# Kernel tuning notes

Measured on AMD Instinct MI355X. Metric: run time of the kernel, lower is better.

The kernel has to match this reference:

```python
import jax, jax.numpy as jnp
import numpy as np
import math

R = 3  # search_radius
GROUPS = 4

def _conv(x, w):
    return jax.lax.conv_general_dilated(x, w, (1, 1), 'SAME',
                                        dimension_numbers=('NCHW', 'OIHW', 'NCHW'))

def _gn(x, g, b, eps=1e-5):
    B, C, H, W = x.shape
    xr = x.reshape(B, GROUPS, C // GROUPS, H, W)
    m = xr.mean(axis=(2, 3, 4), keepdims=True)
    v = xr.var(axis=(2, 3, 4), keepdims=True)
    xn = ((xr - m) * jax.lax.rsqrt(v + eps)).reshape(B, C, H, W)
    return xn * g.reshape(1, C, 1, 1) + b.reshape(1, C, 1, 1)

def _gelu(x):
    return jax.nn.gelu(x, approximate=False)

def _encode(x, W0, Ws, G, Bt):
    x = _gelu(_gn(_conv(x, W0), G[0], Bt[0]))
    for i in range(Ws.shape[0]):  # fixed depth-1 layers
        x = _gelu(_gn(_conv(x, Ws[i]), G[i + 1], Bt[i + 1]))
    return x

def _center_w(h, w):
    y = jnp.linspace(-1.0, 1.0, h)
    x = jnp.linspace(-1.0, 1.0, w)
    yy, xx = jnp.meshgrid(y, x, indexing='ij')
    g = jnp.exp(-(yy ** 2 + xx ** 2) / (2 * 0.5 ** 2))
    return (g / g.sum())[None, None]  # [1,1,H,W]

def _l2n(x):  # F.normalize(dim=1, eps=1e-6)
    n = jnp.sqrt(jnp.sum(x * x, axis=1, keepdims=True))
    return x / jnp.maximum(n, 1e-6)

def setup_inputs() -> dict:
    key = jax.random.key(0)
    ks = jax.random.split(key, 24)
    B, Cr, H, W, Ch, MH = 256, 6, 64, 64, 32, 128
    depth = 4
    feat_dim = Ch * 3 + 2
    s = 0.05
    return {
        'rubin_patch': jax.random.normal(ks[0], (B, Cr, H, W), jnp.float32),
        'vis_patch': jax.random.normal(ks[1], (B, 1, H, W), jnp.float32),
        'pixel_to_sky': jax.random.normal(ks[2], (B, 2, 2), jnp.float32),
        'rW0': jax.random.normal(ks[3], (Ch, Cr, 3, 3), jnp.float32) * s,
        'rWs': jax.random.normal(ks[4], (depth - 1, Ch, Ch, 3, 3), jnp.float32) * s,
        'rG': 1.0 + jax.random.normal(ks[5], (depth, Ch), jnp.float32) * s,
        'rBt': jax.random.normal(ks[6], (depth, Ch), jnp.float32) * s,
        'vW0': jax.random.normal(ks[7], (Ch, 1, 3, 3), jnp.float32) * s,
        'vWs': jax.random.normal(ks[8], (depth - 1, Ch, Ch, 3, 3), jnp.float32) * s,
        'vG': 1.0 + jax.random.normal(ks[9], (depth, Ch), jnp.float32) * s,
        'vBt': jax.random.normal(ks[10], (depth, Ch), jnp.float32) * s,
        'projR': jax.random.normal(ks[11], (Ch, Ch), jnp.float32) * s,
        'projV': jax.random.normal(ks[12], (Ch, Ch), jnp.float32) * s,
        'log_temp': jnp.array(math.log(0.05), jnp.float32),
        'W1': jax.random.normal(ks[13], (feat_dim, MH), jnp.float32) * s,
        'b1': jax.random.normal(ks[14], (MH,), jnp.float32) * s,
        'W2': jax.random.normal(ks[15], (MH, MH), jnp.float32) * s,
        'b2': jax.random.normal(ks[16], (MH,), jnp.float32) * s,
        'W3': jax.random.normal(ks[17], (MH, 3), jnp.float32) * s,
        'b3': jax.random.normal(ks[18], (3,), jnp.float32) * s,
    }

def _forward(rubin_patch, vis_patch, pixel_to_sky, rW0, rWs, rG, rBt,
             vW0, vWs, vG, vBt, projR, projV, log_temp,
             W1, b1, W2, b2, W3, b3):
    rubin_feat = _encode(rubin_patch, rW0, rWs, rG, rBt)  # [B,C,H,W]
    vis_feat = _encode(vis_patch, vW0, vWs, vG, vBt)
    B, C, H, W = rubin_feat.shape

    # --- weighted cross-correlation cost volume ---
    rubin_n = _l2n(jnp.einsum('oc,bchw->bohw', projR, rubin_feat))
    vis_n = _l2n(jnp.einsum('oc,bchw->bohw', projV, vis_feat))
    rubin_energy = jnp.sum(rubin_n * rubin_n, axis=1, keepdims=True)
    gauss = _center_w(H, W)
    sw = rubin_energy * gauss
    sw = sw / (jnp.sum(sw, axis=(2, 3), keepdims=True) + 1e-8)
    rw = rubin_n * sw  # fold weights into rubin features once
    vis_pad = jnp.pad(vis_n, ((0, 0), (0, 0), (R, R), (R, R)), mode='edge')
    scale = 1.0 / math.sqrt(float(C))
    logits = []
    for dy in range(-R, R + 1):
        for dx in range(-R, R + 1):
            sh = vis_pad[:, :, R + dy:R + dy + H, R + dx:R + dx + W]
            logits.append(jnp.sum(rw * sh, axis=(1, 2, 3)) * scale)
    logits = jnp.stack(logits, axis=1)  # [B,(2R+1)^2]

    dx_lut = jnp.array([float(dx) for dy in range(-R, R + 1) for dx in range(-R, R + 1)], jnp.float32)
    dy_lut = jnp.array([float(dy) for dy in range(-R, R + 1) for dx in range(-R, R + 1)], jnp.float32)
    temp = jnp.maximum(jnp.exp(log_temp), 1e-3)
    probs = jax.nn.softmax(logits / temp, axis=1)
    coarse_dx = jnp.sum(probs * dx_lut[None], axis=1)
    coarse_dy = jnp.sum(probs * dy_lut[None], axis=1)

    # --- center-biased pooling + MLP refine ---
    rp = jnp.sum(rubin_feat * gauss, axis=(2, 3))  # [B,C]
    vp = jnp.sum(vis_feat * gauss, axis=(2, 3))
    pooled = jnp.concatenate([rp, vp, rp - vp,
                              jnp.stack([coarse_dx, coarse_dy], axis=1)], axis=1)
    h = _gelu(pooled @ W1 + b1)
    h = _gelu(h @ W2 + b2)
    res = h @ W3 + b3  # [B,3]

    dx_px = coarse_dx + res[:, 0]
    dy_px = coarse_dy + res[:, 1]
    log_sigma = jnp.clip(res[:, 2], -6.0, 3.0)
    pix = jnp.stack([dx_px, dy_px], axis=1)
    pred_sky = jnp.einsum('bij,bj->bi', pixel_to_sky, pix)
    # pack all differentiable outputs: [dx, dy, pred_sky(2), log_sigma, logits(49)]
    return jnp.concatenate([dx_px[:, None], dy_px[:, None], pred_sky,
                            log_sigma[:, None], logits], axis=1)  # [B,54]

def reference(rubin_patch, vis_patch, pixel_to_sky, rW0, rWs, rG, rBt,
              vW0, vWs, vG, vBt, projR, projV, log_temp,
              W1, b1, W2, b2, W3, b3):
    return _forward(rubin_patch, vis_patch, pixel_to_sky, rW0, rWs, rG, rBt,
                    vW0, vWs, vG, vBt, projR, projV, log_temp,
                    W1, b1, W2, b2, W3, b3)
```

## Files before the change

### kernel.cpp

```cpp
#include <hip/hip_runtime.h>
#include <math.h>

#define HW 4096
#define NB 256

typedef __attribute__((ext_vector_type(8))) short bf16x8_t;
typedef __attribute__((ext_vector_type(16))) float f32x16_t;

__device__ __forceinline__ float gelu_f(float x) {
    float z = x * 0.70710678118654752440f;
    float az = fabsf(z);
    float t = 1.0f / fmaf(0.3275911f, az, 1.0f);
    float p = t * fmaf(t, fmaf(t, fmaf(t, fmaf(t, 1.061405429f, -1.453152027f),
                                       1.421413741f), -0.284496736f), 0.254829592f);
    float e = __expf(-az * az);
    float er = 1.0f - p * e;
    er = copysignf(er, z);
    return 0.5f * x * (1.0f + er);
}
__device__ __forceinline__ unsigned short f2bf(float f) {
    unsigned int u = __float_as_uint(f);
    unsigned int r = u + 0x7FFFu + ((u >> 16) & 1u);
    return (unsigned short)(r >> 16);
}
__device__ __forceinline__ float bf2f(unsigned short h) {
    return __uint_as_float(((unsigned int)h) << 16);
}


__global__ __launch_bounds__(256) void gauss_kernel(float* __restrict__ gauss) {
    __shared__ float sg[HW];
    __shared__ float sR[4];
    int tid = threadIdx.x;
    float part = 0.0f;
    for (int p = tid; p < HW; p += 256) {
        int y = p >> 6, x = p & 63;
        float yy = -1.0f + (2.0f / 63.0f) * (float)y;
        float xx = -1.0f + (2.0f / 63.0f) * (float)x;
        float g = expf(-(yy * yy + xx * xx) * 2.0f);
        sg[p] = g;
        part += g;
    }
#pragma unroll
    for (int off = 32; off > 0; off >>= 1) part += __shfl_down(part, off);
    if ((tid & 63) == 0) sR[tid >> 6] = part;
    __syncthreads();
    float invt = 1.0f / (sR[0] + sR[1] + sR[2] + sR[3]);
    for (int p = tid; p < HW; p += 256) gauss[p] = sg[p] * invt;
}

__global__ __launch_bounds__(256) void prep_w_kernel(
    const float* __restrict__ rWs, const float* __restrict__ vWs,
    const float* __restrict__ rW0, const float* __restrict__ vW0,
    const float* __restrict__ projR, const float* __restrict__ projV,
    unsigned short* __restrict__ wq) {
    int i = blockIdx.x * 256 + threadIdx.x;
    if (i >= 119808) return;
    float wv;
    if (i < 110592) {
        int j = i & 7;
        int lane = (i >> 3) & 63;
        int f = i >> 9;
        int hl = f & 1, k2 = (f >> 1) & 1, tap = (f >> 2) % 9, layer = (f >> 2) / 9;
        int co = lane & 31, hf = lane >> 5;
        int ci = k2 * 16 + hf * 8 + j;
        int ky = tap / 3, kx = tap % 3;
        wv = (layer < 3)
            ? rWs[(((size_t)layer * 32 + co) * 32 + ci) * 9 + ky * 3 + kx]
            : vWs[(((size_t)(layer - 3) * 32 + co) * 32 + ci) * 9 + ky * 3 + kx];
        unsigned short h = f2bf(wv);
        unsigned short l = f2bf(wv - bf2f(h));
        wq[i] = hl ? l : h;
        return;
    }
    if (i < 115712) {
        int i2 = i - 110592;
        int j = i2 & 7;
        int lane = (i2 >> 3) & 63;
        int co = lane & 31, hf = lane >> 5;
        if (i2 < 4096) {
            int f = i2 >> 9;
            int hl = f & 1, ks = f >> 1;
            int q = ks * 16 + hf * 8 + j;
            wv = (q < 54) ? rW0[((size_t)co * 6 + q / 9) * 9 + q % 9] : 0.0f;
            unsigned short h = f2bf(wv);
            unsigned short l = f2bf(wv - bf2f(h));
            wq[i] = hl ? l : h;
        } else {
            int i3 = i2 - 4096;
            int f = i3 >> 9;
            int q = hf * 8 + j;
            wv = (q < 9) ? vW0[(size_t)co * 9 + q] : 0.0f;
            unsigned short h = f2bf(wv);
            unsigned short l = f2bf(wv - bf2f(h));
            wq[i] = f ? l : h;
        }
        return;
    }
    int i4 = i - 115712;
    const float* pw = (i4 < 2048) ? projR : projV;
    int r = i4 & 2047;
    int j = r & 7;
    int lane = (r >> 3) & 63;
    int f = r >> 9;
    int hl = f & 1, k2 = f >> 1;
    int co = lane & 31, hf = lane >> 5;
    int ci = k2 * 16 + hf * 8 + j;
    wv = pw[(size_t)co * 32 + ci];
    unsigned short h = f2bf(wv);
    unsigned short l = f2bf(wv - bf2f(h));
    wq[i] = hl ? l : h;
}

template <int CIN>
__global__ __launch_bounds__(128) void conv_first_m_kernel(
    const float* __restrict__ in, const unsigned short* __restrict__ wq0,
    unsigned short* __restrict__ qout, float* __restrict__ statp) {
    constexpr int KQ = CIN * 9;
    constexpr int KS = (KQ + 15) / 16;
    const int b = blockIdx.y;
    const int strip = blockIdx.x;
    const int tid = threadIdx.x;
    const int wv = tid >> 6;
    const int lane = tid & 63;
    const int m = lane & 31;
    const int hf = lane >> 5;
    const int xh32 = wv * 32;

    __shared__ __align__(16) char smem[20736];
    __shared__ float sRed[2][8];
    float* sInF = (float*)smem;

    const int y0 = strip * 4;
    const float* inb = in + (size_t)b * CIN * HW;
    for (int idx = tid; idx < CIN * 6 * 66; idx += 128) {
        int ci = idx / 396;
        int rem = idx - ci * 396;
        int r = rem / 66;
        int col = rem - r * 66;
        int gy = y0 - 1 + r;
        int gx = col - 1;
        float v = 0.0f;
        if (gy >= 0 && gy < 64 && gx >= 0 && gx < 64) v = inb[ci * HW + gy * 64 + gx];
        sInF[ci * 396 + r * 66 + col] = v;
    }

    int P[KS][8];
#pragma unroll
    for (int ks = 0; ks < KS; ++ks)
#pragma unroll
        for (int j = 0; j < 8; ++j) {
            int q = ks * 16 + hf * 8 + j;
            int ci = q / 9, tap = q - ci * 9;
            int ky = tap / 3, kx = tap - ky * 3;
            P[ks][j] = (q < KQ) ? (ci * 396 + ky * 66 + kx) : 0;
        }
    bf16x8_t Wf[KS][2];
#pragma unroll
    for (int ks = 0; ks < KS; ++ks)
#pragma unroll
        for (int hl = 0; hl < 2; ++hl)
            Wf[ks][hl] = __builtin_bit_cast(
                bf16x8_t, *(const uint4*)(wq0 + (size_t)(ks * 2 + hl) * 512 + lane * 8));
    __syncthreads();

    f32x16_t acc[4];
#pragma unroll
    for (int i = 0; i < 4; ++i)
#pragma unroll
        for (int j = 0; j < 16; ++j) acc[i][j] = 0.0f;

    const int xcol = xh32 + m;
#pragma unroll
    for (int orow = 0; orow < 4; ++orow) {
        const int obase = orow * 66 + xcol;
#pragma unroll
        for (int ks = 0; ks < KS; ++ks) {
            unsigned int pk[4];
#pragma unroll
            for (int e = 0; e < 4; ++e) {
                float v0 = sInF[P[ks][e * 2] + obase];
                float v1 = sInF[P[ks][e * 2 + 1] + obase];
                pk[e] = (unsigned)f2bf(v0) | ((unsigned)f2bf(v1) << 16);
            }
            uint4 u; u.x = pk[0]; u.y = pk[1]; u.z = pk[2]; u.w = pk[3];
            bf16x8_t A = __builtin_bit_cast(bf16x8_t, u);
            acc[orow] = __builtin_amdgcn_mfma_f32_32x32x16_bf16(A, Wf[ks][0], acc[orow], 0, 0, 0);
            acc[orow] = __builtin_amdgcn_mfma_f32_32x32x16_bf16(A, Wf[ks][1], acc[orow], 0, 0, 0);
        }
    }

    __syncthreads();
    unsigned short* lds_t = (unsigned short*)smem;
    const int co = lane & 31;
    float s1 = 0.0f, s2 = 0.0f;
#pragma unroll
    for (int orow = 0; orow < 4; ++orow) {
#pragma unroll
        for (int r = 0; r < 16; ++r) {
            int mm = (r & 3) + 8 * (r >> 2) + 4 * hf;
            int pxl = (orow << 6) + xh32 + mm;
            float v = acc[orow][r];
            s1 += v;
            s2 = fmaf(v, v, s2);
            lds_t[pxl * 40 + co] = f2bf(v);
        }
    }
    s1 += __shfl_xor(s1, 32); s2 += __shfl_xor(s2, 32);
    s1 += __shfl_xor(s1, 1);  s2 += __shfl_xor(s2, 1);
    s1 += __shfl_xor(s1, 2);  s2 += __shfl_xor(s2, 2);
    s1 += __shfl_xor(s1, 4);  s2 += __shfl_xor(s2, 4);
    if (lane < 32 && (lane & 7) == 0) {
        sRed[wv][co >> 3] = s1;
        sRed[wv][4 + (co >> 3)] = s2;
    }
    __syncthreads();
    if (tid < 8) statp[((size_t)b * 16 + strip) * 8 + tid] = sRed[0][tid] + sRed[1][tid];

    char* qb = (char*)qout + (size_t)b * 4 * HW * 16;
    const int p0 = y0 * 64;
#pragma unroll
    for (int pi = 0; pi < 2; ++pi) {
        int p = pi * 128 + tid;
#pragma unroll
        for (int s = 0; s < 4; ++s) {
            uint4 uh = *(const uint4*)(lds_t + p * 40 + s * 8);
            *(uint4*)(qb + ((size_t)(s * HW) + p0 + p) * 16) = uh;
        }
    }
}

__global__ __launch_bounds__(256) void gn_finalize_kernel(
    const float* __restrict__ statp, const float* __restrict__ gma,
    const float* __restrict__ bta, float* __restrict__ coef, int n, int ns) {
    int i = blockIdx.x * 256 + threadIdx.x;
    if (i >= n) return;
    int b = i >> 5, c = i & 31, g = c >> 3;
    float s1 = 0.0f, s2 = 0.0f;
    for (int s = 0; s < ns; ++s) {
        s1 += statp[((size_t)b * 16 + s) * 8 + g];
        s2 += statp[((size_t)b * 16 + s) * 8 + 4 + g];
    }
    const float invN = 1.0f / 32768.0f;
    float mean = s1 * invN;
    float var = s2 * invN - mean * mean;
    float rstd = rsqrtf(var + 1e-5f);
    float a = rstd * gma[c];
    float bb = bta[c] - mean * a;
    coef[i * 2 + 0] = a;
    coef[i * 2 + 1] = bb;
}

#define SLOT 80
#define ROWB (66 * SLOT)
__global__ __launch_bounds__(256) void convm_kernel(
    const unsigned short* __restrict__ qin, const float* __restrict__ coef,
    const unsigned short* __restrict__ wq,
    unsigned short* __restrict__ qout, float* __restrict__ statp) {
    const int b = blockIdx.y;
    const int strip = blockIdx.x;
    const int tid = threadIdx.x;
    const int wv = tid >> 6;
    const int lane = tid & 63;
    const int m = lane & 31;
    const int hf = lane >> 5;

    __shared__ __align__(16) char sQ[10 * ROWB];
    __shared__ float sRed[4][8];
    __shared__ float sc[64];

    const int y0 = strip * 8;
    const char* img = (const char*)qin + (size_t)b * 4 * HW * 16;

    if (tid < 64) sc[tid] = coef[b * 64 + tid];
    if (tid < 80) {
        int r = tid >> 3, side = (tid >> 2) & 1, sub = tid & 3;
        uint4 z; z.x = z.y = z.z = z.w = 0;
        *(uint4*)(sQ + r * ROWB + side * 65 * SLOT + sub * 16) = z;
    }
    __syncthreads();

    const int px = tid & 63;
    const int s_id = tid >> 6;
    const int rot = px & 3;
    float ca[8], cb[8];
#pragma unroll
    for (int e = 0; e < 8; ++e) {
        ca[e] = sc[(s_id * 8 + e) * 2 + 0];
        cb[e] = sc[(s_id * 8 + e) * 2 + 1];
    }
    uint4 ld[10];
#pragma unroll
    for (int r = 0; r < 10; ++r) {
        int gy = y0 - 1 + r;
        if (gy >= 0 && gy < 64) {
            ld[r] = *(const uint4*)(img + ((size_t)(s_id * HW) + gy * 64 + px) * 16);
        } else {
            ld[r].x = ld[r].y = ld[r].z = ld[r].w = 0;
        }
    }
    char* dstc = sQ + (px + 1) * SLOT + ((s_id + rot) & 3) * 16;
#pragma unroll
    for (int r = 0; r < 10; ++r) {
        unsigned int hd[4] = {ld[r].x, ld[r].y, ld[r].z, ld[r].w};
        unsigned int ho[4];
#pragma unroll
        for (int e = 0; e < 4; ++e) {
            float x0 = bf2f((unsigned short)(hd[e] & 0xFFFF));
            float x1 = bf2f((unsigned short)(hd[e] >> 16));
            float y0v = gelu_f(fmaf(ca[e * 2], x0, cb[e * 2]));
            float y1v = gelu_f(fmaf(ca[e * 2 + 1], x1, cb[e * 2 + 1]));
            ho[e] = (unsigned)f2bf(y0v) | ((unsigned)f2bf(y1v) << 16);
        }
        uint4 oh; oh.x = ho[0]; oh.y = ho[1]; oh.z = ho[2]; oh.w = ho[3];
        *(uint4*)(dstc + r * ROWB) = oh;
    }
    __syncthreads();

    const int rq = wv & 1;
    const int xh32 = (wv >> 1) * 32;
    f32x16_t acc[4];
#pragma unroll
    for (int i = 0; i < 4; ++i)
#pragma unroll
        for (int j = 0; j < 16; ++j) acc[i][j] = 0.0f;

    for (int kx = 0; kx < 3; ++kx) {
        bf16x8_t Wf[3][2];
#pragma unroll
        for (int ky = 0; ky < 3; ++ky)
#pragma unroll
            for (int k2 = 0; k2 < 2; ++k2) {
                int fi = (((ky * 3 + kx) * 2 + k2) * 2);
                Wf[ky][k2] = __builtin_bit_cast(
                    bf16x8_t, *(const uint4*)(wq + (size_t)fi * 512 + lane * 8));
            }
        const int slotb = xh32 + kx + m;
        const int prot = (m + kx + 3) & 3;
#pragma unroll
        for (int li = 0; li < 6; ++li) {
            const char* rowp = sQ + (rq * 4 + li) * ROWB + slotb * SLOT;
            bf16x8_t Ah[2];
#pragma unroll
            for (int k2 = 0; k2 < 2; ++k2) {
                int s = k2 * 2 + hf;
                Ah[k2] = __builtin_bit_cast(bf16x8_t, *(const uint4*)(rowp + ((s + prot) & 3) * 16));
            }
#pragma unroll
            for (int ky = 0; ky < 3; ++ky) {
                int orow = li - ky;
                if (orow < 0 || orow > 3) continue;
#pragma unroll
                for (int k2 = 0; k2 < 2; ++k2)
                    acc[orow] = __builtin_amdgcn_mfma_f32_32x32x16_bf16(Ah[k2], Wf[ky][k2], acc[orow], 0, 0, 0);
            }
        }
    }

    __syncthreads();
    unsigned short* lds_t = (unsigned short*)sQ;
    const int co = lane & 31;
    float s1 = 0.0f, s2 = 0.0f;
#pragma unroll
    for (int orow = 0; orow < 4; ++orow) {
#pragma unroll
        for (int r = 0; r < 16; ++r) {
            int mm = (r & 3) + 8 * (r >> 2) + 4 * hf;
            int pxl = (rq * 4 + orow) * 64 + xh32 + mm;
            float v = acc[orow][r];
            s1 += v;
            s2 = fmaf(v, v, s2);
            lds_t[pxl * 40 + co] = f2bf(v);
        }
    }
    s1 += __shfl_xor(s1, 32); s2 += __shfl_xor(s2, 32);
    s1 += __shfl_xor(s1, 1);  s2 += __shfl_xor(s2, 1);
    s1 += __shfl_xor(s1, 2);  s2 += __shfl_xor(s2, 2);
    s1 += __shfl_xor(s1, 4);  s2 += __shfl_xor(s2, 4);
    if (lane < 32 && (lane & 7) == 0) {
        sRed[wv][co >> 3] = s1;
        sRed[wv][4 + (co >> 3)] = s2;
    }
    __syncthreads();
    if (tid < 8)
        statp[((size_t)b * 16 + strip) * 8 + tid] =
            sRed[0][tid] + sRed[1][tid] + sRed[2][tid] + sRed[3][tid];

    char* qb = (char*)qout + (size_t)b * 4 * HW * 16;
    const int p0 = y0 * 64;
#pragma unroll
    for (int pi = 0; pi < 2; ++pi) {
        int p = pi * 256 + tid;
#pragma unroll
        for (int s = 0; s < 4; ++s) {
            uint4 uh = *(const uint4*)(lds_t + p * 40 + s * 8);
            *(uint4*)(qb + ((size_t)(s * HW) + p0 + p) * 16) = uh;
        }
    }
}

__global__ __launch_bounds__(256) void proj_kernel(
    const unsigned short* __restrict__ q, const float* __restrict__ coef,
    const unsigned short* __restrict__ wqp, unsigned short* __restrict__ outn,
    float* __restrict__ poolp, float* __restrict__ E, float* __restrict__ swp,
    const float* __restrict__ gauss, int vpad) {
    int b = blockIdx.y, chunk = blockIdx.x, tid = threadIdx.x;
    const int wv = tid >> 6, lane = tid & 63;
    const int ln = lane & 31, hf = lane >> 5;
    __shared__ float sc[64];
    __shared__ float lds_o[256 * 33];
    __shared__ float poolw[4][32];
    __shared__ float sR[4];
    if (tid < 64) sc[tid] = coef[b * 64 + tid];
    __syncthreads();

    const char* qb = (const char*)q + (size_t)b * 4 * HW * 16;
    const int pb0 = chunk * 256 + wv * 64;

    bf16x8_t Bf[2][2];
#pragma unroll
    for (int k2 = 0; k2 < 2; ++k2)
#pragma unroll
        for (int hl = 0; hl < 2; ++hl)
            Bf[k2][hl] = __builtin_bit_cast(
                bf16x8_t, *(const uint4*)(wqp + (size_t)(k2 * 2 + hl) * 512 + lane * 8));

    float psum[2][8];
#pragma unroll
    for (int k2 = 0; k2 < 2; ++k2)
#pragma unroll
        for (int j = 0; j < 8; ++j) psum[k2][j] = 0.0f;

    f32x16_t acc[2];
#pragma unroll
    for (int i = 0; i < 2; ++i)
#pragma unroll
        for (int j = 0; j < 16; ++j) acc[i][j] = 0.0f;

#pragma unroll
    for (int t = 0; t < 2; ++t) {
        int px = pb0 + t * 32 + ln;
        float g = gauss[px];
#pragma unroll
        for (int k2 = 0; k2 < 2; ++k2) {
            int s = k2 * 2 + hf;
            uint4 uh = *(const uint4*)(qb + ((size_t)(s * HW) + px) * 16);
            unsigned int hd[4] = {uh.x, uh.y, uh.z, uh.w};
            unsigned int ah[4], al[4];
#pragma unroll
            for (int e = 0; e < 4; ++e) {
                int c0 = s * 8 + e * 2;
                float x0 = bf2f((unsigned short)(hd[e] & 0xFFFF));
                float x1 = bf2f((unsigned short)(hd[e] >> 16));
                float f0 = gelu_f(fmaf(sc[c0 * 2], x0, sc[c0 * 2 + 1]));
                float f1 = gelu_f(fmaf(sc[c0 * 2 + 2], x1, sc[c0 * 2 + 3]));
                psum[k2][e * 2] = fmaf(f0, g, psum[k2][e * 2]);
                psum[k2][e * 2 + 1] = fmaf(f1, g, psum[k2][e * 2 + 1]);
                unsigned short h0 = f2bf(f0), h1 = f2bf(f1);
                unsigned short l0 = f2bf(f0 - bf2f(h0)), l1 = f2bf(f1 - bf2f(h1));
                ah[e] = (unsigned)h0 | ((unsigned)h1 << 16);
                al[e] = (unsigned)l0 | ((unsigned)l1 << 16);
            }
            uint4 uah; uah.x = ah[0]; uah.y = ah[1]; uah.z = ah[2]; uah.w = ah[3];
            uint4 ual; ual.x = al[0]; ual.y = al[1]; ual.z = al[2]; ual.w = al[3];
            bf16x8_t Ah = __builtin_bit_cast(bf16x8_t, uah);
            bf16x8_t Al = __builtin_bit_cast(bf16x8_t, ual);
            acc[t] = __builtin_amdgcn_mfma_f32_32x32x16_bf16(Ah, Bf[k2][0], acc[t], 0, 0, 0);
            acc[t] = __builtin_amdgcn_mfma_f32_32x32x16_bf16(Ah, Bf[k2][1], acc[t], 0, 0, 0);
            acc[t] = __builtin_amdgcn_mfma_f32_32x32x16_bf16(Al, Bf[k2][0], acc[t], 0, 0, 0);
        }
    }

#pragma unroll
    for (int t = 0; t < 2; ++t)
#pragma unroll
        for (int r = 0; r < 16; ++r) {
            int mm = (r & 3) + 8 * (r >> 2) + 4 * hf;
            lds_o[(wv * 64 + t * 32 + mm) * 33 + ln] = acc[t][r];
        }

#pragma unroll
    for (int k2 = 0; k2 < 2; ++k2)
#pragma unroll
        for (int j = 0; j < 8; ++j) {
            float v = psum[k2][j];
            v += __shfl_xor(v, 1); v += __shfl_xor(v, 2);
            v += __shfl_xor(v, 4); v += __shfl_xor(v, 8);
            v += __shfl_xor(v, 16);
            psum[k2][j] = v;
        }
    if (ln == 0) {
#pragma unroll
        for (int k2 = 0; k2 < 2; ++k2)
#pragma unroll
            for (int j = 0; j < 8; ++j)
                poolw[wv][k2 * 16 + hf * 8 + j] = psum[k2][j];
    }
    __syncthreads();
    if (tid < 32) {
        float s = poolw[0][tid] + poolw[1][tid] + poolw[2][tid] + poolw[3][tid];
        poolp[((size_t)b * 16 + chunk) * 32 + tid] = s;
    }

    int p = chunk * 256 + tid;
    float o[32];
    float nn = 0.0f;
#pragma unroll
    for (int oo = 0; oo < 32; ++oo) {
        o[oo] = lds_o[tid * 33 + oo];
        nn = fmaf(o[oo], o[oo], nn);
    }
    float n = sqrtf(nn);
    float inv = 1.0f / fmaxf(n, 1e-6f);
    if (vpad) {
        int y = p >> 6, x = p & 63;
        unsigned short* vb_ = outn + (size_t)b * 32 * 4608 + y * 72 + x + 4;
#pragma unroll
        for (int oo = 0; oo < 32; ++oo) {
            unsigned short hv = f2bf(o[oo] * inv);
            unsigned short* row = vb_ + (size_t)oo * 4608;
            row[0] = hv;
            if (x == 0) { row[-4] = hv; row[-3] = hv; row[-2] = hv; row[-1] = hv; }
            if (x == 63) { row[1] = hv; row[2] = hv; row[3] = hv; row[4] = hv; }
        }
    } else {
        unsigned short* obp = outn + (size_t)b * 32 * HW + p;
#pragma unroll
        for (int oo = 0; oo < 32; ++oo) obp[(size_t)oo * HW] = f2bf(o[oo] * inv);
    }

    if (E != nullptr) {
        float e = nn * inv * inv;
        E[(size_t)b * HW + p] = e;
        float wvv = e * gauss[p];
#pragma unroll
        for (int off = 32; off > 0; off >>= 1) wvv += __shfl_down(wvv, off);
        if ((tid & 63) == 0) sR[tid >> 6] = wvv;
        __syncthreads();
        if (tid == 0) swp[b * 16 + chunk] = sR[0] + sR[1] + sR[2] + sR[3];
    }
}

__global__ __launch_bounds__(256) void logits_kernel(
    const unsigned short* __restrict__ rn, const unsigned short* __restrict__ vnp,
    const float* __restrict__ E, const float* __restrict__ swp,
    const float* __restrict__ gauss, float* __restrict__ lgpart) {
    int b = blockIdx.x, cg = blockIdx.y, tid = threadIdx.x;
    __shared__ float sR[4][49];
    float acc[49];
#pragma unroll
    for (int k = 0; k < 49; ++k) acc[k] = 0.0f;
    float ssum = 0.0f;
#pragma unroll
    for (int i = 0; i < 16; ++i) ssum += swp[b * 16 + i];
    const float scale = 0.17677669529663688f / (ssum + 1e-8f);
    const int x0 = (tid & 7) * 8;
    const float* Eb = E + (size_t)b * HW;
#pragma unroll 1
    for (int half = 0; half < 2; ++half) {
        const int y = half * 32 + (tid >> 3);
        const int pbase = y * 64 + x0;
        float4 e0 = *(const float4*)(Eb + pbase);
        float4 e1 = *(const float4*)(Eb + pbase + 4);
        float4 g0 = *(const float4*)(gauss + pbase);
        float4 g1 = *(const float4*)(gauss + pbase + 4);
        float qw[8];
        qw[0] = e0.x * g0.x * scale; qw[1] = e0.y * g0.y * scale;
        qw[2] = e0.z * g0.z * scale; qw[3] = e0.w * g0.w * scale;
        qw[4] = e1.x * g1.x * scale; qw[5] = e1.y * g1.y * scale;
        qw[6] = e1.z * g1.z * scale; qw[7] = e1.w * g1.w * scale;
#pragma unroll 1
        for (int cc = 0; cc < 4; ++cc) {
            int c = cg * 4 + cc;
            const unsigned short* rb = rn + ((size_t)b * 32 + c) * HW;
            uint4 rv = *(const uint4*)(rb + pbase);
            unsigned int rd[4] = {rv.x, rv.y, rv.z, rv.w};
            float r_[8];
            r_[0] = bf2f((unsigned short)(rd[0] & 0xFFFF)) * qw[0];
            r_[1] = bf2f((unsigned short)(rd[0] >> 16)) * qw[1];
            r_[2] = bf2f((unsigned short)(rd[1] & 0xFFFF)) * qw[2];
            r_[3] = bf2f((unsigned short)(rd[1] >> 16)) * qw[3];
            r_[4] = bf2f((unsigned short)(rd[2] & 0xFFFF)) * qw[4];
            r_[5] = bf2f((unsigned short)(rd[2] >> 16)) * qw[5];
            r_[6] = bf2f((unsigned short)(rd[3] & 0xFFFF)) * qw[6];
            r_[7] = bf2f((unsigned short)(rd[3] >> 16)) * qw[7];
            const unsigned short* vplane = vnp + ((size_t)b * 32 + c) * 4608;
#pragma unroll
            for (int dy = 0; dy < 7; ++dy) {
                int ry = y + dy - 3;
                ry = ry < 0 ? 0 : (ry > 63 ? 63 : ry);
                const unsigned short* vp = vplane + ry * 72 + x0;
                uint4 va = *(const uint4*)vp;
                uint4 vb2 = *(const uint4*)(vp + 8);
                unsigned int vd[8] = {va.x, va.y, va.z, va.w, vb2.x, vb2.y, vb2.z, vb2.w};
                float v[16];
#pragma unroll
                for (int j2 = 0; j2 < 8; ++j2) {
                    v[j2 * 2] = bf2f((unsigned short)(vd[j2] & 0xFFFF));
                    v[j2 * 2 + 1] = bf2f((unsigned short)(vd[j2] >> 16));
                }
#pragma unroll
                for (int dx = 0; dx < 7; ++dx)
#pragma unroll
                    for (int j = 0; j < 8; ++j)
                        acc[dy * 7 + dx] = fmaf(r_[j], v[j + dx + 1], acc[dy * 7 + dx]);
            }
        }
    }
#pragma unroll
    for (int k = 0; k < 49; ++k) {
#pragma unroll
        for (int off = 32; off > 0; off >>= 1) acc[k] += __shfl_down(acc[k], off);
    }
    int wid = tid >> 6;
    if ((tid & 63) == 0) {
#pragma unroll
        for (int k = 0; k < 49; ++k) sR[wid][k] = acc[k];
    }
    __syncthreads();
    if (tid < 49)
        lgpart[((size_t)b * 8 + cg) * 49 + tid] =
            sR[0][tid] + sR[1][tid] + sR[2][tid] + sR[3][tid];
}

__global__ __launch_bounds__(128) void head_kernel(
    const float* __restrict__ lg, const float* __restrict__ rpp,
    const float* __restrict__ vpp, const float* __restrict__ p2s,
    const float* __restrict__ log_temp,
    const float* __restrict__ W1, const float* __restrict__ b1,
    const float* __restrict__ W2, const float* __restrict__ b2,
    const float* __restrict__ W3, const float* __restrict__ b3,
    float* __restrict__ out) {
    int b = blockIdx.x, t = threadIdx.x;
    __shared__ float slg[49];
    __shared__ float pooled[98];
    __shared__ float h1[128], h2[128];
    __shared__ float cxy[2];
    __shared__ float res[3];
    const float* lgp = lg + (size_t)b * 8 * 49;
    if (t < 49) {
        float s = 0.0f;
#pragma unroll
        for (int g = 0; g < 8; ++g) s += lgp[g * 49 + t];
        slg[t] = s;
    }
    __syncthreads();
    if (t == 0) {
        float temp = fmaxf(expf(log_temp[0]), 0.001f);
        float invT = 1.0f / temp;
        float m = -1e30f;
        for (int k = 0; k < 49; ++k) m = fmaxf(m, slg[k] * invT);
        float s = 0.0f, pdx = 0.0f, pdy = 0.0f;
        for (int k = 0; k < 49; ++k) {
            float e = expf(slg[k] * invT - m);
            s += e;
            pdx += e * (float)((k % 7) - 3);
            pdy += e * (float)((k / 7) - 3);
        }
        cxy[0] = pdx / s;
        cxy[1] = pdy / s;
    }
    __syncthreads();
    if (t < 32) {
        float a = 0.0f, c = 0.0f;
#pragma unroll
        for (int k = 0; k < 16; ++k) {
            a += rpp[((size_t)b * 16 + k) * 32 + t];
            c += vpp[((size_t)b * 16 + k) * 32 + t];
        }
        pooled[t] = a;
        pooled[32 + t] = c;
        pooled[64 + t] = a - c;
    }
    if (t == 0) {
        pooled[96] = cxy[0];
        pooled[97] = cxy[1];
    }
    __syncthreads();
    float s1 = b1[t];
    for (int i = 0; i < 98; ++i) s1 = fmaf(pooled[i], W1[i * 128 + t], s1);
    h1[t] = gelu_f(s1);
    __syncthreads();
    float s2 = b2[t];
    for (int i = 0; i < 128; ++i) s2 = fmaf(h1[i], W2[i * 128 + t], s2);
    h2[t] = gelu_f(s2);
    __syncthreads();
    if (t < 3) {
        float r = b3[t];
        for (int i = 0; i < 128; ++i) r = fmaf(h2[i], W3[i * 3 + t], r);
        res[t] = r;
    }
    __syncthreads();
    if (t == 0) {
        float dxp = cxy[0] + res[0];
        float dyp = cxy[1] + res[1];
        float ls = fminf(fmaxf(res[2], -6.0f), 3.0f);
        const float* M = p2s + b * 4;
        float* ob = out + b * 54;
        ob[0] = dxp;
        ob[1] = dyp;
        ob[2] = M[0] * dxp + M[1] * dyp;
        ob[3] = M[2] * dxp + M[3] * dyp;
        ob[4] = ls;
    }
    if (t < 49) out[b * 54 + 5 + t] = slg[t];
}

extern "C" void kernel_launch(void* const* d_in, const int* in_sizes, int n_in,
                              void* d_out, int out_size, void* d_ws, size_t ws_size,
                              hipStream_t stream) {
    (void)in_sizes; (void)n_in; (void)out_size;
    const float* rubin = (const float*)d_in[0];
    const float* vis   = (const float*)d_in[1];
    const float* p2s   = (const float*)d_in[2];
    const float* rW0   = (const float*)d_in[3];
    const float* rWs   = (const float*)d_in[4];
    const float* rG    = (const float*)d_in[5];
    const float* rBt   = (const float*)d_in[6];
    const float* vW0   = (const float*)d_in[7];
    const float* vWs   = (const float*)d_in[8];
    const float* vG    = (const float*)d_in[9];
    const float* vBt   = (const float*)d_in[10];
    const float* projR = (const float*)d_in[11];
    const float* projV = (const float*)d_in[12];
    const float* logT  = (const float*)d_in[13];
    const float* W1    = (const float*)d_in[14];
    const float* b1    = (const float*)d_in[15];
    const float* W2    = (const float*)d_in[16];
    const float* b2    = (const float*)d_in[17];
    const float* W3    = (const float*)d_in[18];
    const float* b3    = (const float*)d_in[19];
    float* out = (float*)d_out;

    char* ws = (char*)d_ws;
    size_t off = 0;
    unsigned short* vnB = (unsigned short*)(ws + off); off += (size_t)NB * 32 * 4608 * 2;
    float* gauss  = (float*)(ws + off); off += HW * 4;
    float* statp  = (float*)(ws + off); off += (size_t)NB * 16 * 8 * 4;
    float* coefS  = (float*)(ws + off); off += (size_t)NB * 64 * 4;
    float* swp    = (float*)(ws + off); off += (size_t)NB * 16 * 4;
    float* rpp    = (float*)(ws + off); off += (size_t)NB * 16 * 32 * 4;
    float* vpp    = (float*)(ws + off); off += (size_t)NB * 16 * 32 * 4;
    float* lgbuf  = (float*)(ws + off); off += (size_t)NB * 8 * 49 * 4;
    unsigned short* wq = (unsigned short*)(ws + off); off += 119808ull * 2;
    off = (off + 255) & ~(size_t)255;
    const size_t fixed_bytes = off;
    const size_t perb = 2ull * HW * 64 + HW * 4;
    int BC = 1;
    if (ws_size > fixed_bytes + perb) {
        size_t t = (ws_size - fixed_bytes) / perb;
        BC = t > (size_t)NB ? NB : (int)t;
    }
    unsigned short* Q1 = (unsigned short*)(ws + off);
    unsigned short* Q2 = (unsigned short*)(ws + off + (size_t)BC * HW * 64);
    float* E = (float*)(ws + off + 2ull * BC * HW * 64);
    unsigned short* wq0r = wq + 110592;
    unsigned short* wq0v = wq + 114688;
    unsigned short* wqpR = wq + 115712;
    unsigned short* wqpV = wq + 117760;

    dim3 blk256(256), blk128(128);
    gauss_kernel<<<1, 256, 0, stream>>>(gauss);
    prep_w_kernel<<<468, 256, 0, stream>>>(rWs, vWs, rW0, vW0, projR, projV, wq);

    for (int b0 = 0; b0 < NB; b0 += BC) {
        const int bc = (NB - b0) < BC ? (NB - b0) : BC;
        dim3 cg16(16, bc), cg8(8, bc);
        const int gnblk = (bc * 32 + 255) / 256;
        float* sp = statp + (size_t)b0 * 128;
        float* cS = coefS + (size_t)b0 * 64;

        conv_first_m_kernel<1><<<cg16, blk128, 0, stream>>>(vis + (size_t)b0 * HW, wq0v, Q1, sp);
        gn_finalize_kernel<<<gnblk, 256, 0, stream>>>(sp, vG + 0, vBt + 0, cS, bc * 32, 16);
        convm_kernel<<<cg8, blk256, 0, stream>>>(Q1, cS, wq + 3 * 18432, Q2, sp);
        gn_finalize_kernel<<<gnblk, 256, 0, stream>>>(sp, vG + 32, vBt + 32, cS, bc * 32, 8);
        convm_kernel<<<cg8, blk256, 0, stream>>>(Q2, cS, wq + 4 * 18432, Q1, sp);
        gn_finalize_kernel<<<gnblk, 256, 0, stream>>>(sp, vG + 64, vBt + 64, cS, bc * 32, 8);
        convm_kernel<<<cg8, blk256, 0, stream>>>(Q1, cS, wq + 5 * 18432, Q2, sp);
        gn_finalize_kernel<<<gnblk, 256, 0, stream>>>(sp, vG + 96, vBt + 96, cS, bc * 32, 8);
        proj_kernel<<<cg16, blk256, 0, stream>>>(Q2, cS, wqpV, vnB + (size_t)b0 * 32 * 4608,
                                                 vpp + (size_t)b0 * 512,
                                                 (float*)nullptr, (float*)nullptr, gauss, 1);
    }

    for (int b0 = 0; b0 < NB; b0 += BC) {
        const int bc = (NB - b0) < BC ? (NB - b0) : BC;
        dim3 cg16(16, bc), cg8(8, bc);
        const int gnblk = (bc * 32 + 255) / 256;
        float* sp = statp + (size_t)b0 * 128;
        float* cS = coefS + (size_t)b0 * 64;
        float* sw = swp + (size_t)b0 * 16;
        unsigned short* rnB = Q1;

        conv_first_m_kernel<6><<<cg16, blk128, 0, stream>>>(rubin + (size_t)b0 * 6 * HW, wq0r, Q1, sp);
        gn_finalize_kernel<<<gnblk, 256, 0, stream>>>(sp, rG + 0, rBt + 0, cS, bc * 32, 16);
        convm_kernel<<<cg8, blk256, 0, stream>>>(Q1, cS, wq + 0 * 18432, Q2, sp);
        gn_finalize_kernel<<<gnblk, 256, 0, stream>>>(sp, rG + 32, rBt + 32, cS, bc * 32, 8);
        convm_kernel<<<cg8, blk256, 0, stream>>>(Q2, cS, wq + 1 * 18432, Q1, sp);
        gn_finalize_kernel<<<gnblk, 256, 0, stream>>>(sp, rG + 64, rBt + 64, cS, bc * 32, 8);
        convm_kernel<<<cg8, blk256, 0, stream>>>(Q1, cS, wq + 2 * 18432, Q2, sp);
        gn_finalize_kernel<<<gnblk, 256, 0, stream>>>(sp, rG + 96, rBt + 96, cS, bc * 32, 8);
        proj_kernel<<<cg16, blk256, 0, stream>>>(Q2, cS, wqpR, rnB,
                                                 rpp + (size_t)b0 * 512, E, sw, gauss, 0);
        logits_kernel<<<dim3(bc, 8), blk256, 0, stream>>>(rnB, vnB + (size_t)b0 * 32 * 4608,
                                                          E, sw, gauss,
                                                          lgbuf + (size_t)b0 * 8 * 49);
    }

    head_kernel<<<NB, 128, 0, stream>>>(lgbuf, rpp, vpp, p2s, logT, W1, b1, W2, b2, W3, b3, out);
}
```

Baseline: 726.7 us.

## Batch rubin and vis encoder stages into shared launches via grid z

Merges the two encoder branches so each conv, group-norm finalize and projection stage runs for both branches in one launch, using blockIdx.z to pick the branch. This halves the number of launches and doubles the grid per launch, which should fill the GPU better. The gauss kernel is folded into the weight-prep kernel as an extra block, and the logits kernel is split into 16 channel groups instead of 8 for more parallelism. The cost is double the workspace per batch chunk, and the first conv is no longer templated, so its loop bounds are only known at runtime.

```diff
diff --git a/kernel.cpp b/kernel.cpp
--- a/kernel.cpp
+++ b/kernel.cpp
@@ -28,32 +28,32 @@
 }
 
 
-__global__ __launch_bounds__(256) void gauss_kernel(float* __restrict__ gauss) {
-    __shared__ float sg[HW];
-    __shared__ float sR[4];
-    int tid = threadIdx.x;
-    float part = 0.0f;
-    for (int p = tid; p < HW; p += 256) {
-        int y = p >> 6, x = p & 63;
-        float yy = -1.0f + (2.0f / 63.0f) * (float)y;
-        float xx = -1.0f + (2.0f / 63.0f) * (float)x;
-        float g = expf(-(yy * yy + xx * xx) * 2.0f);
-        sg[p] = g;
-        part += g;
-    }
-#pragma unroll
-    for (int off = 32; off > 0; off >>= 1) part += __shfl_down(part, off);
-    if ((tid & 63) == 0) sR[tid >> 6] = part;
-    __syncthreads();
-    float invt = 1.0f / (sR[0] + sR[1] + sR[2] + sR[3]);
-    for (int p = tid; p < HW; p += 256) gauss[p] = sg[p] * invt;
-}
-
 __global__ __launch_bounds__(256) void prep_w_kernel(
     const float* __restrict__ rWs, const float* __restrict__ vWs,
     const float* __restrict__ rW0, const float* __restrict__ vW0,
     const float* __restrict__ projR, const float* __restrict__ projV,
-    unsigned short* __restrict__ wq) {
+    unsigned short* __restrict__ wq, float* __restrict__ gauss) {
+    if (blockIdx.x == 468) {
+        __shared__ float sg[HW];
+        __shared__ float sR[4];
+        int tid = threadIdx.x;
+        float part = 0.0f;
+        for (int p = tid; p < HW; p += 256) {
+            int y = p >> 6, x = p & 63;
+            float yy = -1.0f + (2.0f / 63.0f) * (float)y;
+            float xx = -1.0f + (2.0f / 63.0f) * (float)x;
+            float g = expf(-(yy * yy + xx * xx) * 2.0f);
+            sg[p] = g;
+            part += g;
+        }
+#pragma unroll
+        for (int off = 32; off > 0; off >>= 1) part += __shfl_down(part, off);
+        if ((tid & 63) == 0) sR[tid >> 6] = part;
+        __syncthreads();
+        float invt = 1.0f / (sR[0] + sR[1] + sR[2] + sR[3]);
+        for (int p = tid; p < HW; p += 256) gauss[p] = sg[p] * invt;
+        return;
+    }
     int i = blockIdx.x * 256 + threadIdx.x;
     if (i >= 119808) return;
     float wv;
@@ -112,12 +112,20 @@
     wq[i] = hl ? l : h;
 }
 
-template <int CIN>
-__global__ __launch_bounds__(128) void conv_first_m_kernel(
-    const float* __restrict__ in, const unsigned short* __restrict__ wq0,
-    unsigned short* __restrict__ qout, float* __restrict__ statp) {
-    constexpr int KQ = CIN * 9;
-    constexpr int KS = (KQ + 15) / 16;
+__global__ __launch_bounds__(128) void conv_first2_kernel(
+    const float* __restrict__ inR, const float* __restrict__ inV,
+    const unsigned short* __restrict__ wq0r, const unsigned short* __restrict__ wq0v,
+    unsigned short* __restrict__ qoutR, unsigned short* __restrict__ qoutV,
+    float* __restrict__ statpR, float* __restrict__ statpV) {
+    const int z = blockIdx.z;
+    const float* in = z ? inV : inR;
+    const unsigned short* wq0 = z ? wq0v : wq0r;
+    unsigned short* qout = z ? qoutV : qoutR;
+    float* statp = z ? statpV : statpR;
+    const int CIN = z ? 1 : 6;
+    const int KQ = CIN * 9;
+    const int KSr = z ? 1 : 4;
+
     const int b = blockIdx.y;
     const int strip = blockIdx.x;
     const int tid = threadIdx.x;
@@ -133,7 +141,7 @@
 
     const int y0 = strip * 4;
     const float* inb = in + (size_t)b * CIN * HW;
-    for (int idx = tid; idx < CIN * 6 * 66; idx += 128) {
+    for (int idx = tid; idx < CIN * 396; idx += 128) {
         int ci = idx / 396;
         int rem = idx - ci * 396;
         int r = rem / 66;
@@ -145,9 +153,9 @@
         sInF[ci * 396 + r * 66 + col] = v;
     }
 
-    int P[KS][8];
-#pragma unroll
-    for (int ks = 0; ks < KS; ++ks)
+    int P[4][8];
+#pragma unroll
+    for (int ks = 0; ks < 4; ++ks)
 #pragma unroll
         for (int j = 0; j < 8; ++j) {
             int q = ks * 16 + hf * 8 + j;
@@ -155,13 +163,14 @@
             int ky = tap / 3, kx = tap - ky * 3;
             P[ks][j] = (q < KQ) ? (ci * 396 + ky * 66 + kx) : 0;
         }
-    bf16x8_t Wf[KS][2];
-#pragma unroll
-    for (int ks = 0; ks < KS; ++ks)
-#pragma unroll
-        for (int hl = 0; hl < 2; ++hl)
-            Wf[ks][hl] = __builtin_bit_cast(
-                bf16x8_t, *(const uint4*)(wq0 + (size_t)(ks * 2 + hl) * 512 + lane * 8));
+    bf16x8_t Wf[4][2];
+#pragma unroll
+    for (int ks = 0; ks < 4; ++ks)
+        if (ks < KSr)
+#pragma unroll
+            for (int hl = 0; hl < 2; ++hl)
+                Wf[ks][hl] = __builtin_bit_cast(
+                    bf16x8_t, *(const uint4*)(wq0 + (size_t)(ks * 2 + hl) * 512 + lane * 8));
     __syncthreads();
 
     f32x16_t acc[4];
@@ -175,7 +184,8 @@
     for (int orow = 0; orow < 4; ++orow) {
         const int obase = orow * 66 + xcol;
 #pragma unroll
-        for (int ks = 0; ks < KS; ++ks) {
+        for (int ks = 0; ks < 4; ++ks) {
+            if (ks >= KSr) continue;
             unsigned int pk[4];
 #pragma unroll
             for (int e = 0; e < 4; ++e) {
@@ -230,11 +240,16 @@
     }
 }
 
-__global__ __launch_bounds__(256) void gn_finalize_kernel(
-    const float* __restrict__ statp, const float* __restrict__ gma,
-    const float* __restrict__ bta, float* __restrict__ coef, int n, int ns) {
+__global__ __launch_bounds__(256) void gn2_kernel(
+    const float* __restrict__ statpR, const float* __restrict__ gR,
+    const float* __restrict__ bR, float* __restrict__ coefR,
+    const float* __restrict__ statpV, const float* __restrict__ gV,
+    const float* __restrict__ bV, float* __restrict__ coefV, int n, int ns) {
     int i = blockIdx.x * 256 + threadIdx.x;
-    if (i >= n) return;
+    if (i >= 2 * n) return;
+    const float* statp; const float* gma; const float* bta; float* coef;
+    if (i < n) { statp = statpR; gma = gR; bta = bR; coef = coefR; }
+    else { i -= n; statp = statpV; gma = gV; bta = bV; coef = coefV; }
     int b = i >> 5, c = i & 31, g = c >> 3;
     float s1 = 0.0f, s2 = 0.0f;
     for (int s = 0; s < ns; ++s) {
@@ -253,10 +268,19 @@
 
 #define SLOT 80
 #define ROWB (66 * SLOT)
-__global__ __launch_bounds__(256) void convm_kernel(
-    const unsigned short* __restrict__ qin, const float* __restrict__ coef,
-    const unsigned short* __restrict__ wq,
-    unsigned short* __restrict__ qout, float* __restrict__ statp) {
+__global__ __launch_bounds__(256) void convm2_kernel(
+    const unsigned short* __restrict__ qinR, const unsigned short* __restrict__ qinV,
+    const float* __restrict__ coefR, const float* __restrict__ coefV,
+    const unsigned short* __restrict__ wqR, const unsigned short* __restrict__ wqV,
+    unsigned short* __restrict__ qoutR, unsigned short* __restrict__ qoutV,
+    float* __restrict__ statpR, float* __restrict__ statpV) {
+    const int z = blockIdx.z;
+    const unsigned short* qin = z ? qinV : qinR;
+    const float* coef = z ? coefV : coefR;
+    const unsigned short* wq = z ? wqV : wqR;
+    unsigned short* qout = z ? qoutV : qoutR;
+    float* statp = z ? statpV : statpR;
+
     const int b = blockIdx.y;
     const int strip = blockIdx.x;
     const int tid = threadIdx.x;
@@ -275,8 +299,8 @@
     if (tid < 64) sc[tid] = coef[b * 64 + tid];
     if (tid < 80) {
         int r = tid >> 3, side = (tid >> 2) & 1, sub = tid & 3;
-        uint4 z; z.x = z.y = z.z = z.w = 0;
-        *(uint4*)(sQ + r * ROWB + side * 65 * SLOT + sub * 16) = z;
+        uint4 zv; zv.x = zv.y = zv.z = zv.w = 0;
+        *(uint4*)(sQ + r * ROWB + side * 65 * SLOT + sub * 16) = zv;
     }
     __syncthreads();
 
@@ -399,11 +423,21 @@
     }
 }
 
-__global__ __launch_bounds__(256) void proj_kernel(
-    const unsigned short* __restrict__ q, const float* __restrict__ coef,
-    const unsigned short* __restrict__ wqp, unsigned short* __restrict__ outn,
-    float* __restrict__ poolp, float* __restrict__ E, float* __restrict__ swp,
-    const float* __restrict__ gauss, int vpad) {
+__global__ __launch_bounds__(256) void proj2_kernel(
+    const unsigned short* __restrict__ qR, const unsigned short* __restrict__ qV,
+    const float* __restrict__ coefR, const float* __restrict__ coefV,
+    const unsigned short* __restrict__ wqpR, const unsigned short* __restrict__ wqpV,
+    unsigned short* __restrict__ outR, unsigned short* __restrict__ outV,
+    float* __restrict__ rpp, float* __restrict__ vpp,
+    float* __restrict__ E, float* __restrict__ swp,
+    const float* __restrict__ gauss) {
+    const int z = blockIdx.z;
+    const unsigned short* q = z ? qV : qR;
+    const float* coef = z ? coefV : coefR;
+    const unsigned short* wqp = z ? wqpV : wqpR;
+    unsigned short* outn = z ? outV : outR;
+    float* poolp = z ? vpp : rpp;
+
     int b = blockIdx.y, chunk = blockIdx.x, tid = threadIdx.x;
     const int wv = tid >> 6, lane = tid & 63;
     const int ln = lane & 31, hf = lane >> 5;
@@ -512,7 +546,7 @@
     }
     float n = sqrtf(nn);
     float inv = 1.0f / fmaxf(n, 1e-6f);
-    if (vpad) {
+    if (z) {
         int y = p >> 6, x = p & 63;
         unsigned short* vb_ = outn + (size_t)b * 32 * 4608 + y * 72 + x + 4;
 #pragma unroll
@@ -529,7 +563,7 @@
         for (int oo = 0; oo < 32; ++oo) obp[(size_t)oo * HW] = f2bf(o[oo] * inv);
     }
 
-    if (E != nullptr) {
+    if (!z) {
         float e = nn * inv * inv;
         E[(size_t)b * HW + p] = e;
         float wvv = e * gauss[p];
@@ -570,8 +604,8 @@
         qw[4] = e1.x * g1.x * scale; qw[5] = e1.y * g1.y * scale;
         qw[6] = e1.z * g1.z * scale; qw[7] = e1.w * g1.w * scale;
 #pragma unroll 1
-        for (int cc = 0; cc < 4; ++cc) {
-            int c = cg * 4 + cc;
+        for (int cc = 0; cc < 2; ++cc) {
+            int c = cg * 2 + cc;
             const unsigned short* rb = rn + ((size_t)b * 32 + c) * HW;
             uint4 rv = *(const uint4*)(rb + pbase);
             unsigned int rd[4] = {rv.x, rv.y, rv.z, rv.w};
@@ -619,7 +653,7 @@
     }
     __syncthreads();
     if (tid < 49)
-        lgpart[((size_t)b * 8 + cg) * 49 + tid] =
+        lgpart[((size_t)b * 16 + cg) * 49 + tid] =
             sR[0][tid] + sR[1][tid] + sR[2][tid] + sR[3][tid];
 }
 
@@ -637,11 +671,11 @@
     __shared__ float h1[128], h2[128];
     __shared__ float cxy[2];
     __shared__ float res[3];
-    const float* lgp = lg + (size_t)b * 8 * 49;
+    const float* lgp = lg + (size_t)b * 16 * 49;
     if (t < 49) {
         float s = 0.0f;
 #pragma unroll
-        for (int g = 0; g < 8; ++g) s += lgp[g * 49 + t];
+        for (int g = 0; g < 16; ++g) s += lgp[g * 49 + t];
         slg[t] = s;
     }
     __syncthreads();
@@ -735,76 +769,76 @@
     char* ws = (char*)d_ws;
     size_t off = 0;
     unsigned short* vnB = (unsigned short*)(ws + off); off += (size_t)NB * 32 * 4608 * 2;
-    float* gauss  = (float*)(ws + off); off += HW * 4;
-    float* statp  = (float*)(ws + off); off += (size_t)NB * 16 * 8 * 4;
-    float* coefS  = (float*)(ws + off); off += (size_t)NB * 64 * 4;
-    float* swp    = (float*)(ws + off); off += (size_t)NB * 16 * 4;
-    float* rpp    = (float*)(ws + off); off += (size_t)NB * 16 * 32 * 4;
-    float* vpp    = (float*)(ws + off); off += (size_t)NB * 16 * 32 * 4;
-    float* lgbuf  = (float*)(ws + off); off += (size_t)NB * 8 * 49 * 4;
+    float* gauss   = (float*)(ws + off); off += HW * 4;
+    float* statpR  = (float*)(ws + off); off += (size_t)NB * 16 * 8 * 4;
+    float* statpV  = (float*)(ws + off); off += (size_t)NB * 16 * 8 * 4;
+    float* coefR   = (float*)(ws + off); off += (size_t)NB * 64 * 4;
+    float* coefV   = (float*)(ws + off); off += (size_t)NB * 64 * 4;
+    float* swp     = (float*)(ws + off); off += (size_t)NB * 16 * 4;
+    float* rpp     = (float*)(ws + off); off += (size_t)NB * 16 * 32 * 4;
+    float* vpp     = (float*)(ws + off); off += (size_t)NB * 16 * 32 * 4;
+    float* lgbuf   = (float*)(ws + off); off += (size_t)NB * 16 * 49 * 4;
     unsigned short* wq = (unsigned short*)(ws + off); off += 119808ull * 2;
     off = (off + 255) & ~(size_t)255;
     const size_t fixed_bytes = off;
-    const size_t perb = 2ull * HW * 64 + HW * 4;
+    const size_t perb = 4ull * HW * 64 + HW * 4;
     int BC = 1;
     if (ws_size > fixed_bytes + perb) {
         size_t t = (ws_size - fixed_bytes) / perb;
         BC = t > (size_t)NB ? NB : (int)t;
     }
-    unsigned short* Q1 = (unsigned short*)(ws + off);
-    unsigned short* Q2 = (unsigned short*)(ws + off + (size_t)BC * HW * 64);
-    float* E = (float*)(ws + off + 2ull * BC * HW * 64);
+    unsigned short* Q1r = (unsigned short*)(ws + off);
+    unsigned short* Q2r = (unsigned short*)(ws + off + 1ull * BC * HW * 64);
+    unsigned short* Q1v = (unsigned short*)(ws + off + 2ull * BC * HW * 64);
+    unsigned short* Q2v = (unsigned short*)(ws + off + 3ull * BC * HW * 64);
+    float* E = (float*)(ws + off + 4ull * BC * HW * 64);
     unsigned short* wq0r = wq + 110592;
     unsigned short* wq0v = wq + 114688;
     unsigned short* wqpR = wq + 115712;
     unsigned short* wqpV = wq + 117760;
 
     dim3 blk256(256), blk128(128);
-    gauss_kernel<<<1, 256, 0, stream>>>(gauss);
-    prep_w_kernel<<<468, 256, 0, stream>>>(rWs, vWs, rW0, vW0, projR, projV, wq);
+    prep_w_kernel<<<469, 256, 0, stream>>>(rWs, vWs, rW0, vW0, projR, projV, wq, gauss);
 
     for (int b0 = 0; b0 < NB; b0 += BC) {
         const int bc = (NB - b0) < BC ? (NB - b0) : BC;
-        dim3 cg16(16, bc), cg8(8, bc);
-        const int gnblk = (bc * 32 + 255) / 256;
-        float* sp = statp + (size_t)b0 * 128;
-        float* cS = coefS + (size_t)b0 * 64;
-
-        conv_first_m_kernel<1><<<cg16, blk128, 0, stream>>>(vis + (size_t)b0 * HW, wq0v, Q1, sp);
-        gn_finalize_kernel<<<gnblk, 256, 0, stream>>>(sp, vG + 0, vBt + 0, cS, bc * 32, 16);
-        convm_kernel<<<cg8, blk256, 0, stream>>>(Q1, cS, wq + 3 * 18432, Q2, sp);
-        gn_finalize_kernel<<<gnblk, 256, 0, stream>>>(sp, vG + 32, vBt + 32, cS, bc * 32, 8);
-        convm_kernel<<<cg8, blk256, 0, stream>>>(Q2, cS, wq + 4 * 18432, Q1, sp);
-        gn_finalize_kernel<<<gnblk, 256, 0, stream>>>(sp, vG + 64, vBt + 64, cS, bc * 32, 8);
-        convm_kernel<<<cg8, blk256, 0, stream>>>(Q1, cS, wq + 5 * 18432, Q2, sp);
-        gn_finalize_kernel<<<gnblk, 256, 0, stream>>>(sp, vG + 96, vBt + 96, cS, bc * 32, 8);
-        proj_kernel<<<cg16, blk256, 0, stream>>>(Q2, cS, wqpV, vnB + (size_t)b0 * 32 * 4608,
-                                                 vpp + (size_t)b0 * 512,
-                                                 (float*)nullptr, (float*)nullptr, gauss, 1);
-    }
-
-    for (int b0 = 0; b0 < NB; b0 += BC) {
-        const int bc = (NB - b0) < BC ? (NB - b0) : BC;
-        dim3 cg16(16, bc), cg8(8, bc);
-        const int gnblk = (bc * 32 + 255) / 256;
-        float* sp = statp + (size_t)b0 * 128;
-        float* cS = coefS + (size_t)b0 * 64;
+        dim3 cg16(16, bc, 2), cg8(8, bc, 2);
+        const int gnblk = (2 * bc * 32 + 255) / 256;
+        float* spR = statpR + (size_t)b0 * 128;
+        float* spV = statpV + (size_t)b0 * 128;
+        float* cR = coefR + (size_t)b0 * 64;
+        float* cV = coefV + (size_t)b0 * 64;
         float* sw = swp + (size_t)b0 * 16;
-        unsigned short* rnB = Q1;
-
-        conv_first_m_kernel<6><<<cg16, blk128, 0, stream>>>(rubin + (size_t)b0 * 6 * HW, wq0r, Q1, sp);
-        gn_finalize_kernel<<<gnblk, 256, 0, stream>>>(sp, rG + 0, rBt + 0, cS, bc * 32, 16);
-        convm_kernel<<<cg8, blk256, 0, stream>>>(Q1, cS, wq + 0 * 18432, Q2, sp);
-        gn_finalize_kernel<<<gnblk, 256, 0, stream>>>(sp, rG + 32, rBt + 32, cS, bc * 32, 8);
-        convm_kernel<<<cg8, blk256, 0, stream>>>(Q2, cS, wq + 1 * 18432, Q1, sp);
-        gn_finalize_kernel<<<gnblk, 256, 0, stream>>>(sp, rG + 64, rBt + 64, cS, bc * 32, 8);
-        convm_kernel<<<cg8, blk256, 0, stream>>>(Q1, cS, wq + 2 * 18432, Q2, sp);
-        gn_finalize_kernel<<<gnblk, 256, 0, stream>>>(sp, rG + 96, rBt + 96, cS, bc * 32, 8);
-        proj_kernel<<<cg16, blk256, 0, stream>>>(Q2, cS, wqpR, rnB,
-                                                 rpp + (size_t)b0 * 512, E, sw, gauss, 0);
-        logits_kernel<<<dim3(bc, 8), blk256, 0, stream>>>(rnB, vnB + (size_t)b0 * 32 * 4608,
-                                                          E, sw, gauss,
-                                                          lgbuf + (size_t)b0 * 8 * 49);
+        unsigned short* rnB = Q1r;
+
+        conv_first2_kernel<<<cg16, blk128, 0, stream>>>(
+            rubin + (size_t)b0 * 6 * HW, vis + (size_t)b0 * HW, wq0r, wq0v,
+            Q1r, Q1v, spR, spV);
+        gn2_kernel<<<gnblk, 256, 0, stream>>>(spR, rG + 0, rBt + 0, cR,
+                                              spV, vG + 0, vBt + 0, cV, bc * 32, 16);
+        convm2_kernel<<<cg8, blk256, 0, stream>>>(Q1r, Q1v, cR, cV,
+                                                  wq + 0 * 18432, wq + 3 * 18432,
+                                                  Q2r, Q2v, spR, spV);
+        gn2_kernel<<<gnblk, 256, 0, stream>>>(spR, rG + 32, rBt + 32, cR,
+                                              spV, vG + 32, vBt + 32, cV, bc * 32, 8);
+        convm2_kernel<<<cg8, blk256, 0, stream>>>(Q2r, Q2v, cR, cV,
+                                                  wq + 1 * 18432, wq + 4 * 18432,
+                                                  Q1r, Q1v, spR, spV);
+        gn2_kernel<<<gnblk, 256, 0, stream>>>(spR, rG + 64, rBt + 64, cR,
+                                              spV, vG + 64, vBt + 64, cV, bc * 32, 8);
+        convm2_kernel<<<cg8, blk256, 0, stream>>>(Q1r, Q1v, cR, cV,
+                                                  wq + 2 * 18432, wq + 5 * 18432,
+                                                  Q2r, Q2v, spR, spV);
+        gn2_kernel<<<gnblk, 256, 0, stream>>>(spR, rG + 96, rBt + 96, cR,
+                                              spV, vG + 96, vBt + 96, cV, bc * 32, 8);
+        proj2_kernel<<<cg16, blk256, 0, stream>>>(Q2r, Q2v, cR, cV, wqpR, wqpV,
+                                                  rnB, vnB + (size_t)b0 * 32 * 4608,
+                                                  rpp + (size_t)b0 * 512,
+                                                  vpp + (size_t)b0 * 512,
+                                                  E, sw, gauss);
+        logits_kernel<<<dim3(bc, 16), blk256, 0, stream>>>(
+            rnB, vnB + (size_t)b0 * 32 * 4608, E, sw, gauss,
+            lgbuf + (size_t)b0 * 16 * 49);
     }
 
     head_kernel<<<NB, 128, 0, stream>>>(lgbuf, rpp, vpp, p2s, logT, W1, b1, W2, b2, W3, b3, out);
```

New measurement: 760.3 us. 1.05x slower.
